# Kernel tuning notes

Measured on AMD Instinct MI355X. Metric: run time of the kernel, lower is better.

The kernel has to match this reference:

```python
import jax, jax.numpy as jnp
import numpy as np

N, DEG, FIN, FOUT, K = 50000, 16, 32, 64, 3
E = N * DEG


def setup_inputs() -> dict:
    key = jax.random.key(0)
    ks = jax.random.split(key, 10)
    rng = np.random.default_rng(0)
    # unique edges sorted row-major (src*N+dst), ring guarantees deg_in/out>0
    ring = np.arange(N, dtype=np.int64) * N + (np.arange(N, dtype=np.int64) + 1) % N
    cand = np.unique(rng.integers(0, N * N, size=3 * E, dtype=np.int64))
    cand = np.setdiff1d(cand, ring, assume_unique=True)[: E - N]
    codes = np.sort(np.concatenate([cand, ring]))
    assert codes.shape[0] == E
    edge_index = jnp.asarray(np.stack([codes // N, codes % N]).astype(np.int32))
    X = jax.random.normal(ks[0], (N, FIN), jnp.float32)
    edge_weight = jax.random.uniform(ks[1], (E,), jnp.float32, 0.5, 1.5)
    cin = FIN + FOUT
    xav = float(np.sqrt(6.0 / (cin + FOUT)))
    def w(k):
        return jax.random.uniform(k, (2, K, cin, FOUT), jnp.float32, -xav, xav)
    return {
        'X': X, 'edge_index': edge_index, 'edge_weight': edge_weight,
        'Wz': w(ks[2]), 'bz': jnp.zeros((FOUT,), jnp.float32),
        'Wr': w(ks[3]), 'br': jnp.zeros((FOUT,), jnp.float32),
        'Wh': w(ks[4]), 'bh': jnp.zeros((FOUT,), jnp.float32),
    }


def _dconv(X, src, dst, rev_src, rev_dst, norm_out, norm_in, W, b):
    n = X.shape[0]
    def prop(x, s, d, nrm):  # out[d] += nrm * x[s]
        return jax.ops.segment_sum(nrm[:, None] * x[s], d, num_segments=n)
    H = X @ W[0, 0] + X @ W[1, 0]
    if W.shape[1] > 1:
        Tx1o = prop(X, src, dst, norm_out)
        Tx1i = prop(X, rev_src, rev_dst, norm_in)
        H = H + Tx1o @ W[0, 1] + Tx1i @ W[1, 1]
        for k in range(2, W.shape[1]):
            Tx1o = 2.0 * prop(Tx1o, src, dst, norm_out) - X
            Tx1i = 2.0 * prop(Tx1i, rev_src, rev_dst, norm_in) - X
            H = H + Tx1o @ W[0, k] + Tx1i @ W[1, k]
    return H + b


def reference(X, edge_index, edge_weight, Wz, bz, Wr, br, Wh, bh):
    n = X.shape[0]
    src, dst = edge_index[0], edge_index[1]
    deg_out = jax.ops.segment_sum(edge_weight, src, num_segments=n)
    deg_in = jax.ops.segment_sum(edge_weight, dst, num_segments=n)
    # faithful to original: both norms indexed by row (source)
    norm_out = 1.0 / deg_out[src]
    norm_in = 1.0 / deg_in[src]
    # reverse edges in dense_to_sparse(adj.T) order: sorted by (dst, src)
    order = jnp.argsort(dst.astype(jnp.int64) * n + src.astype(jnp.int64))
    rev_src, rev_dst = dst[order], src[order]
    H = jnp.zeros((n, Wz.shape[-1]), X.dtype)
    dc = lambda inp, W, b: _dconv(inp, src, dst, rev_src, rev_dst, norm_out, norm_in, W, b)
    Z = jax.nn.sigmoid(dc(jnp.concatenate([X, H], axis=1), Wz, bz))
    R = jax.nn.sigmoid(dc(jnp.concatenate([X, H], axis=1), Wr, br))
    H_tilde = jnp.tanh(dc(jnp.concatenate([X, H * R], axis=1), Wh, bh))
    return Z * H + (1.0 - Z) * H_tilde
```

## Files before the change

kernel.cpp:

```cpp
#include <hip/hip_runtime.h>
#include <hip/hip_fp16.h>
#include <cmath>

#define NN 50000
#define NE 800000
#define PADF 96
#define NBIN 196
#define NBLK 391
#define FCAP 6144
#define DST_HI 42949
#define SRC_CUT 33648

__device__ __forceinline__ unsigned short f2h(float f) {
  __half h = __float2half_rn(f);
  return *reinterpret_cast<unsigned short*>(&h);
}

typedef _Float16 half4 __attribute__((ext_vector_type(4)));
typedef float f32x4 __attribute__((ext_vector_type(4)));

__global__ __launch_bounds__(256) void k_aux(const float* __restrict__ X, const int* __restrict__ src,
                                             const int* __restrict__ dst, const float* __restrict__ ew,
                                             int* __restrict__ H,
                                             int* __restrict__ rptr, float* __restrict__ dout,
                                             const float* __restrict__ Wz, const float* __restrict__ Wh,
                                             unsigned short* __restrict__ WT, unsigned short* __restrict__ Xh) {
  __shared__ int hh[256];
  int bid = blockIdx.x;
  int t = threadIdx.x;
  if (bid >= 667) {
    int h = bid - 667;
    hh[t] = 0;
    __syncthreads();
#pragma unroll
    for (int r = 0; r < 8; ++r) {
      int e = h * 2048 + r * 256 + t;
      if (e < NE) atomicAdd(&hh[dst[e] >> 8], 1);
    }
    __syncthreads();
    if (t < NBIN) H[t * NBLK + h] = hh[t];
  } else if (bid < 196) {
    int i = bid * 256 + t;
    if (i >= NN) return;
    int lo = 0, hi = NE;
    while (lo < hi) { int m = (lo + hi) >> 1; if (src[m] < i) lo = m + 1; else hi = m; }
    int lo2 = lo, hi2 = NE;
    while (lo2 < hi2) { int m = (lo2 + hi2) >> 1; if (src[m] < i + 1) lo2 = m + 1; else hi2 = m; }
    rptr[i] = lo;
    if (i == NN - 1) rptr[NN] = lo2;
    float a = 0.f;
    for (int p = lo; p < lo2; ++p) a += ew[p];
    dout[i] = a;
  } else if (bid < 276) {
    int idx = (bid - 196) * 256 + t;
    int kk = idx >> 7, f = idx & 127;
    int blk = kk >> 5, c = kk & 31;
    const float* W = (f < 64) ? Wz : Wh;
    int fl = f & 63;
    float v;
    if (blk == 0)      v = W[c * 64 + fl] + W[18432 + c * 64 + fl];
    else if (blk == 1) v = W[6144 + c * 64 + fl];
    else if (blk == 2) v = W[18432 + 6144 + c * 64 + fl];
    else if (blk == 3) v = W[2 * 6144 + c * 64 + fl];
    else               v = W[18432 + 2 * 6144 + c * 64 + fl];
    WT[f * 160 + kk] = f2h(v);
  } else {
    int tt = (bid - 276) * 256 + t;
    int base = tt * 16;
    if (base >= NN * 32) return;
#pragma unroll
    for (int q = 0; q < 2; ++q) {
      const float4 a = *(const float4*)&X[base + q * 8];
      const float4 b = *(const float4*)&X[base + q * 8 + 4];
      ushort4 o1 = make_ushort4(f2h(a.x), f2h(a.y), f2h(a.z), f2h(a.w));
      ushort4 o2 = make_ushort4(f2h(b.x), f2h(b.y), f2h(b.z), f2h(b.w));
      *(ushort4*)&Xh[base + q * 8] = o1;
      *(ushort4*)&Xh[base + q * 8 + 4] = o2;
    }
  }
}

__global__ __launch_bounds__(512) void k_scanrow(int* __restrict__ H, int* __restrict__ rowtot) {
  __shared__ int tmp[512];
  int row = blockIdx.x;
  int t = threadIdx.x;
  int v = (t < NBLK) ? H[row * NBLK + t] : 0;
  tmp[t] = v;
  __syncthreads();
  for (int off = 1; off < 512; off <<= 1) {
    int u = (t >= (unsigned)off) ? tmp[t - off] : 0;
    __syncthreads();
    tmp[t] += u;
    __syncthreads();
  }
  if (t < NBLK) H[row * NBLK + t] = tmp[t] - v;
  if (t == 511) rowtot[row] = tmp[511];
}

__global__ __launch_bounds__(256) void k_part(const int* __restrict__ src, const int* __restrict__ dst,
                                              const int* __restrict__ P, const int* __restrict__ rowtot,
                                              unsigned long long* __restrict__ cmp64) {
  __shared__ int loc[NBIN];
  __shared__ int rs[256];
  __shared__ int rbase[NBIN];
  int h = blockIdx.x;
  int t = threadIdx.x;
  int v = (t < NBIN) ? rowtot[t] : 0;
  rs[t] = v;
  if (t < NBIN) loc[t] = 0;
  __syncthreads();
  for (int off = 1; off < 256; off <<= 1) {
    int u = (t >= (unsigned)off) ? rs[t - off] : 0;
    __syncthreads();
    rs[t] += u;
    __syncthreads();
  }
  if (t < NBIN) rbase[t] = rs[t] - v;
  __syncthreads();
#pragma unroll
  for (int r = 0; r < 8; ++r) {
    int e = h * 2048 + r * 256 + t;
    if (e < NE) {
      int d = dst[e];
      int bin = d >> 8;
      int rk = atomicAdd(&loc[bin], 1);
      int pos = rbase[bin] + P[bin * NBLK + h] + rk;
      cmp64[pos] = ((unsigned long long)(d & 255) << 48) |
                   ((unsigned long long)src[e] << 24) | (unsigned long long)e;
    }
  }
}

__global__ __launch_bounds__(1024) void k_fine(const int* __restrict__ rowtot, const float* __restrict__ ew,
                                               const unsigned long long* __restrict__ cmp64,
                                               int2* __restrict__ cmp, int* __restrict__ sp,
                                               float* __restrict__ din) {
  __shared__ unsigned long long a1[FCAP], a2[FCAP];
  __shared__ int fh[256], fcnt[256], fo[257];
  __shared__ int bs[2];
  int cb = blockIdx.x;
  int t = threadIdx.x;
  if (t < 64) {
    int s = 0;
    for (int i = t; i < cb; i += 64) s += rowtot[i];
    s += __shfl_xor(s, 32, 64); s += __shfl_xor(s, 16, 64); s += __shfl_xor(s, 8, 64);
    s += __shfl_xor(s, 4, 64);  s += __shfl_xor(s, 2, 64);  s += __shfl_xor(s, 1, 64);
    if (t == 0) { bs[0] = s; bs[1] = s + rowtot[cb]; }
  }
  if (t < 256) { fh[t] = 0; fcnt[t] = 0; }
  __syncthreads();
  int base = bs[0];
  int m = bs[1] - base;
  if (m > FCAP) m = FCAP;
  for (int i = t; i < m; i += 1024) {
    unsigned long long it = cmp64[base + i];
    a1[i] = it;
    atomicAdd(&fh[(int)(it >> 48)], 1);
  }
  __syncthreads();
  if (t < 64) {
    int v0 = fh[t * 4], v1 = fh[t * 4 + 1], v2 = fh[t * 4 + 2], v3 = fh[t * 4 + 3];
    int s1 = v0 + v1, s2 = s1 + v2, tot = s2 + v3;
    int run = tot;
    for (int off = 1; off < 64; off <<= 1) {
      int v = __shfl_up(run, off, 64);
      if (t >= off) run += v;
    }
    int excl = run - tot;
    fo[t * 4] = excl; fo[t * 4 + 1] = excl + v0; fo[t * 4 + 2] = excl + s1; fo[t * 4 + 3] = excl + s2;
    if (t == 63) fo[256] = excl + tot;
  }
  __syncthreads();
  for (int i = t; i < m; i += 1024) {
    unsigned long long it = a1[i];
    int b = (int)(it >> 48);
    int p2 = fo[b] + atomicAdd(&fcnt[b], 1);
    a2[p2] = it;
  }
  __syncthreads();
  for (int i = t; i < m; i += 1024) {
    unsigned long long it = a2[i];
    cmp[base + i] = make_int2((int)(it & 0xFFFFFF), (int)((it >> 24) & 0xFFFF));
  }
  if (t < 256) {
    int d = cb * 256 + t;
    if (d <= NN) sp[d] = base + fo[t];
  }
  {
    int d = cb * 256 + t;
    if (t < 257 && d == NN) sp[NN] = base + fo[t];
  }
  int nd = t >> 2, ln = t & 3;
  int d = cb * 256 + nd;
  if (d < NN) {
    float s = 0.f;
    int e0 = fo[nd], e1 = fo[nd + 1];
    for (int i = e0 + ln; i < e1; i += 4) s += ew[(int)(a2[i] & 0xFFFFFF)];
    s += __shfl_down(s, 2, 4);
    s += __shfl_down(s, 1, 4);
    if (ln == 0) din[d] = s;
  }
}

__global__ __launch_bounds__(256) void k_sortw(const int* __restrict__ sp, const int2* __restrict__ cmp,
                                               const int* __restrict__ rawsrc,
                                               const float* __restrict__ dout, const float* __restrict__ din,
                                               int2* __restrict__ cnf, int2* __restrict__ cnr) {
  __shared__ int s0s;
  {
    int t = threadIdx.x;
    if (t < 64) {
      int b0h = sp[DST_HI];
      int nh = sp[DST_HI + 1] - b0h;
      int c = 0;
      for (int i = t; i < nh; i += 64) c += (cmp[b0h + i].y < SRC_CUT);
      c += __shfl_xor(c, 32, 64); c += __shfl_xor(c, 16, 64); c += __shfl_xor(c, 8, 64);
      c += __shfl_xor(c, 4, 64);  c += __shfl_xor(c, 2, 64);  c += __shfl_xor(c, 1, 64);
      if (t == 0) s0s = b0h + c;
    }
  }
  __syncthreads();
  int wv = (blockIdx.x * 256 + threadIdx.x) >> 6;
  int lane = threadIdx.x & 63;
  if (wv >= NN) return;
  int b0 = sp[wv], b1 = sp[wv + 1];
  int n = b1 - b0;
  int s0 = s0s;
  if (n > 64) {
    if (lane == 0) {
      int es[PADF], ss[PADF];
      int nn = n > PADF ? PADF : n;
      for (int i = 0; i < nn; ++i) { int2 pe = cmp[b0 + i]; es[i] = pe.x; ss[i] = pe.y; }
      for (int i = 1; i < nn; ++i) {
        int ve = es[i], vs = ss[i]; int j = i - 1;
        while (j >= 0 && es[j] > ve) { es[j + 1] = es[j]; ss[j + 1] = ss[j]; --j; }
        es[j + 1] = ve; ss[j + 1] = vs;
      }
      for (int i = 0; i < nn; ++i) {
        int vs = ss[i];
        cnf[b0 + i] = make_int2(vs, __float_as_int(1.0f / dout[vs]));
        int j = b0 + i - s0; if (j < 0) j += NE;
        cnr[es[i]] = make_int2(wv, __float_as_int(1.0f / din[rawsrc[j]]));
      }
    }
    return;
  }
  unsigned long long k = ~0ULL;
  if (lane < n) {
    int2 pe = cmp[b0 + lane];
    k = ((unsigned long long)(unsigned)pe.x << 32) | (unsigned)pe.y;
  }
  if (n > 1) {
#pragma unroll
    for (int kk = 2; kk <= 64; kk <<= 1) {
#pragma unroll
      for (int j = kk >> 1; j > 0; j >>= 1) {
        unsigned long long o = __shfl_xor(k, j, 64);
        bool lower = (lane & j) == 0;
        bool asc = (lane & kk) == 0;
        bool keepmin = (lower == asc);
        if (keepmin ? (o < k) : (o > k)) k = o;
      }
    }
  }
  if (lane < n) {
    int ve = (int)(k >> 32);
    int vs = (int)(k & 0xffffffffu);
    cnf[b0 + lane] = make_int2(vs, __float_as_int(1.0f / dout[vs]));
    int j = b0 + lane - s0; if (j < 0) j += NE;
    cnr[ve] = make_int2(wv, __float_as_int(1.0f / din[rawsrc[j]]));
  }
}

__global__ __launch_bounds__(256) void k_prop2(const unsigned short* __restrict__ inA, const int* __restrict__ rpA,
                                               const int2* __restrict__ cnA, float* __restrict__ outA,
                                               unsigned short* __restrict__ outAh,
                                               const unsigned short* __restrict__ inB, const int* __restrict__ rpB,
                                               const int2* __restrict__ cnB, float* __restrict__ outB,
                                               unsigned short* __restrict__ outBh,
                                               const float* __restrict__ sub, float mul) {
  int t = blockIdx.x * 256 + threadIdx.x;
  const int half = NN * 8;
  const unsigned short* in; const int* rp; const int2* cn; float* out; unsigned short* outh;
  if (t < half) { in = inA; rp = rpA; cn = cnA; out = outA; outh = outAh; }
  else          { in = inB; rp = rpB; cn = cnB; out = outB; outh = outBh; t -= half; }
  int r = t >> 3;
  if (r >= NN) return;
  int lane8 = t & 7;
  int c4 = lane8 * 4;
  int b = rp[r], e2 = rp[r + 1];
  float a0[4] = {0.f, 0.f, 0.f, 0.f}, a1[4] = {0.f, 0.f, 0.f, 0.f};
  int p = b;
#define GATH(cc, ww) { \
    uint2 bv = *(const uint2*)&in[(cc) * 32 + c4]; \
    float2 f01 = __half22float2(*(const __half2*)&bv.x); \
    float2 f23 = __half22float2(*(const __half2*)&bv.y); \
    float* a = (jj & 1) ? a1 : a0; \
    a[0] += (ww) * f01.x; a[1] += (ww) * f01.y; \
    a[2] += (ww) * f23.x; a[3] += (ww) * f23.y; }
  for (; p + 16 <= e2; p += 16) {
    int2 u = cn[p + lane8];
    int2 v = cn[p + 8 + lane8];
#pragma unroll
    for (int jj = 0; jj < 8; ++jj) {
      int col = __shfl(u.x, jj, 8);
      float w = __int_as_float(__shfl(u.y, jj, 8));
      GATH(col, w)
    }
#pragma unroll
    for (int jj = 0; jj < 8; ++jj) {
      int col = __shfl(v.x, jj, 8);
      float w = __int_as_float(__shfl(v.y, jj, 8));
      GATH(col, w)
    }
  }
  for (; p + 8 <= e2; p += 8) {
    int2 u = cn[p + lane8];
#pragma unroll
    for (int jj = 0; jj < 8; ++jj) {
      int col = __shfl(u.x, jj, 8);
      float w = __int_as_float(__shfl(u.y, jj, 8));
      GATH(col, w)
    }
  }
  for (int jj = 0; p < e2; ++p) {
    int2 c1 = cn[p];
    float w = __int_as_float(c1.y);
    GATH(c1.x, w)
  }
#undef GATH
  float ax = a0[0] + a1[0], ay = a0[1] + a1[1], az = a0[2] + a1[2], aw = a0[3] + a1[3];
  float4 o;
  if (sub) {
    const float4 s = *(const float4*)&sub[r * 32 + c4];
    o.x = mul * ax - s.x; o.y = mul * ay - s.y; o.z = mul * az - s.z; o.w = mul * aw - s.w;
  } else {
    o.x = ax; o.y = ay; o.z = az; o.w = aw;
  }
  if (out) *(float4*)&out[r * 32 + c4] = o;
  if (outh) {
    ushort4 oh = make_ushort4(f2h(o.x), f2h(o.y), f2h(o.z), f2h(o.w));
    *(ushort4*)&outh[r * 32 + c4] = oh;
  }
}

__global__ __launch_bounds__(256) void k_gemm(const unsigned short* __restrict__ Xh,
                                              const unsigned short* __restrict__ T1oh,
                                              const unsigned short* __restrict__ T1ih,
                                              const unsigned short* __restrict__ T2oh,
                                              const unsigned short* __restrict__ T2ih,
                                              const unsigned short* __restrict__ WT,
                                              const float* __restrict__ bz, const float* __restrict__ bh,
                                              float* __restrict__ out) {
  __shared__ unsigned short wlds[128 * 168];
  const int tid = threadIdx.x;
  for (int i = tid; i < 128 * 20; i += 256) {
    int n = i / 20, o = i % 20;
    *(uint4*)&wlds[n * 168 + o * 8] = *(const uint4*)&WT[n * 160 + o * 8];
  }
  __syncthreads();
  const int l = tid & 63, wid = tid >> 6;
  const int m0 = wid * 16;
  const int rb = blockIdx.x * 64;
  int grow = rb + m0 + (l & 15); if (grow >= NN) grow = NN - 1;
  const int kg = (l >> 4) * 4;
  f32x4 acc[8];
#pragma unroll
  for (int t = 0; t < 8; ++t) acc[t] = (f32x4){0.f, 0.f, 0.f, 0.f};
  const unsigned short* srcs[5] = {Xh, T1oh, T1ih, T2oh, T2ih};
#pragma unroll
  for (int s = 0; s < 5; ++s) {
    const unsigned short* A = srcs[s];
#pragma unroll
    for (int h2 = 0; h2 < 2; ++h2) {
      const int kk = h2 * 16;
      half4 af = *(const half4*)&A[grow * 32 + kk + kg];
      const int kglob = s * 32 + kk + kg;
#pragma unroll
      for (int t = 0; t < 8; ++t) {
        half4 bf = *(const half4*)&wlds[(t * 16 + (l & 15)) * 168 + kglob];
        acc[t] = __builtin_amdgcn_mfma_f32_16x16x16f16(af, bf, acc[t], 0, 0, 0);
      }
    }
  }
  const int c = l & 15;
#pragma unroll
  for (int t = 0; t < 4; ++t) {
    int col = t * 16 + c;
    float bzv = bz[col], bhv = bh[col];
#pragma unroll
    for (int i = 0; i < 4; ++i) {
      int r = rb + m0 + (l >> 4) * 4 + i;
      if (r < NN) {
        float z = 1.f / (1.f + expf(-(acc[t][i] + bzv)));
        float hv = tanhf(acc[t + 4][i] + bhv);
        out[r * 64 + col] = (1.f - z) * hv;
      }
    }
  }
}

extern "C" void kernel_launch(void* const* d_in, const int* in_sizes, int n_in,
                              void* d_out, int out_size, void* d_ws, size_t ws_size,
                              hipStream_t stream) {
  const float* X  = (const float*)d_in[0];
  const int*   ei = (const int*)d_in[1];
  const float* ew = (const float*)d_in[2];
  const float* Wz = (const float*)d_in[3];
  const float* bz = (const float*)d_in[4];
  const float* Wh = (const float*)d_in[7];
  const float* bh = (const float*)d_in[8];
  float* out = (float*)d_out;
  const int* src = ei;
  const int* dst = ei + NE;

  char* p = (char*)d_ws;
  auto alloc = [&](size_t bytes) -> char* {
    char* r = p;
    p += (bytes + 255) & ~(size_t)255;
    return r;
  };
  unsigned short* Xh   = (unsigned short*)alloc((size_t)NN * 32 * 2);
  unsigned short* T1oh = (unsigned short*)alloc((size_t)NN * 32 * 2);
  unsigned short* T1ih = (unsigned short*)alloc((size_t)NN * 32 * 2);
  unsigned short* T2oh = (unsigned short*)alloc((size_t)NN * 32 * 2);
  unsigned short* T2ih = (unsigned short*)alloc((size_t)NN * 32 * 2);
  unsigned long long* cmp64 = (unsigned long long*)alloc((size_t)NE * 8);
  int2*  cmp     = (int2*)alloc((size_t)NE * 8);
  int2*  cnf     = (int2*)alloc((size_t)NE * 8);
  int2*  cnr     = (int2*)alloc((size_t)NE * 8);
  int*   H       = (int*)alloc((size_t)NBIN * NBLK * 4);
  int*   rowtot  = (int*)alloc(NBIN * 4);
  int*   sp      = (int*)alloc((NN + 1) * 4);
  int*   rptr    = (int*)alloc((NN + 1) * 4);
  float* dout    = (float*)alloc(NN * 4);
  float* din     = (float*)alloc(NN * 4);
  unsigned short* WT = (unsigned short*)alloc(128 * 160 * 2);

  k_aux<<<1058, 256, 0, stream>>>(X, src, dst, ew, H, rptr, dout, Wz, Wh, WT, Xh);
  k_scanrow<<<NBIN, 512, 0, stream>>>(H, rowtot);
  k_part<<<NBLK, 256, 0, stream>>>(src, dst, H, rowtot, cmp64);
  k_fine<<<NBIN, 1024, 0, stream>>>(rowtot, ew, cmp64, cmp, sp, din);
  k_sortw<<<12500, 256, 0, stream>>>(sp, cmp, src, dout, din, cnf, cnr);

  k_prop2<<<3125, 256, 0, stream>>>(Xh, sp, cnf, nullptr, T1oh,
                                    Xh, rptr, cnr, nullptr, T1ih, nullptr, 1.f);
  k_prop2<<<3125, 256, 0, stream>>>(T1oh, sp, cnf, nullptr, T2oh,
                                    T1ih, rptr, cnr, nullptr, T2ih, X, 2.f);

  k_gemm<<<782, 256, 0, stream>>>(Xh, T1oh, T1ih, T2oh, T2ih, WT, bz, bh, out);
}
```

Baseline: 233.4 us.

## Fuse per-destination edge sort into k_fine and defer in-degree reciprocal to propagation

```diff
diff --git a/kernel.cpp b/kernel.cpp
--- a/kernel.cpp
+++ b/kernel.cpp
@@ -24,21 +24,32 @@
                                              int* __restrict__ H,
                                              int* __restrict__ rptr, float* __restrict__ dout,
                                              const float* __restrict__ Wz, const float* __restrict__ Wh,
-                                             unsigned short* __restrict__ WT, unsigned short* __restrict__ Xh) {
+                                             unsigned short* __restrict__ WT, unsigned short* __restrict__ Xh,
+                                             int* __restrict__ s0g) {
   __shared__ int hh[256];
+  __shared__ int s0l;
   int bid = blockIdx.x;
   int t = threadIdx.x;
   if (bid >= 667) {
     int h = bid - 667;
     hh[t] = 0;
-    __syncthreads();
+    if (t == 0) s0l = 0;
+    __syncthreads();
+    int my = 0;
 #pragma unroll
     for (int r = 0; r < 8; ++r) {
       int e = h * 2048 + r * 256 + t;
-      if (e < NE) atomicAdd(&hh[dst[e] >> 8], 1);
-    }
+      if (e < NE) {
+        int d = dst[e];
+        atomicAdd(&hh[d >> 8], 1);
+        my += (d < DST_HI) ? 1 : 0;
+        my += (d == DST_HI && src[e] < SRC_CUT) ? 1 : 0;
+      }
+    }
+    atomicAdd(&s0l, my);
     __syncthreads();
     if (t < NBIN) H[t * NBLK + h] = hh[t];
+    if (t == 0) atomicAdd(s0g, s0l);
   } else if (bid < 196) {
     int i = bid * 256 + t;
     if (i >= NN) return;
@@ -133,8 +144,10 @@
 
 __global__ __launch_bounds__(1024) void k_fine(const int* __restrict__ rowtot, const float* __restrict__ ew,
                                                const unsigned long long* __restrict__ cmp64,
-                                               int2* __restrict__ cmp, int* __restrict__ sp,
-                                               float* __restrict__ din) {
+                                               const int* __restrict__ rawsrc, const float* __restrict__ dout,
+                                               const int* __restrict__ s0g,
+                                               int* __restrict__ sp, float* __restrict__ din,
+                                               int2* __restrict__ cnf, int2* __restrict__ cnr) {
   __shared__ unsigned long long a1[FCAP], a2[FCAP];
   __shared__ int fh[256], fcnt[256], fo[257];
   __shared__ int bs[2];
@@ -177,11 +190,6 @@
     int p2 = fo[b] + atomicAdd(&fcnt[b], 1);
     a2[p2] = it;
   }
-  __syncthreads();
-  for (int i = t; i < m; i += 1024) {
-    unsigned long long it = a2[i];
-    cmp[base + i] = make_int2((int)(it & 0xFFFFFF), (int)((it >> 24) & 0xFFFF));
-  }
   if (t < 256) {
     int d = cb * 256 + t;
     if (d <= NN) sp[d] = base + fo[t];
@@ -190,100 +198,82 @@
     int d = cb * 256 + t;
     if (t < 257 && d == NN) sp[NN] = base + fo[t];
   }
-  int nd = t >> 2, ln = t & 3;
-  int d = cb * 256 + nd;
-  if (d < NN) {
-    float s = 0.f;
-    int e0 = fo[nd], e1 = fo[nd + 1];
-    for (int i = e0 + ln; i < e1; i += 4) s += ew[(int)(a2[i] & 0xFFFFFF)];
-    s += __shfl_down(s, 2, 4);
-    s += __shfl_down(s, 1, 4);
-    if (ln == 0) din[d] = s;
-  }
-}
-
-__global__ __launch_bounds__(256) void k_sortw(const int* __restrict__ sp, const int2* __restrict__ cmp,
-                                               const int* __restrict__ rawsrc,
-                                               const float* __restrict__ dout, const float* __restrict__ din,
-                                               int2* __restrict__ cnf, int2* __restrict__ cnr) {
-  __shared__ int s0s;
-  {
-    int t = threadIdx.x;
-    if (t < 64) {
-      int b0h = sp[DST_HI];
-      int nh = sp[DST_HI + 1] - b0h;
-      int c = 0;
-      for (int i = t; i < nh; i += 64) c += (cmp[b0h + i].y < SRC_CUT);
-      c += __shfl_xor(c, 32, 64); c += __shfl_xor(c, 16, 64); c += __shfl_xor(c, 8, 64);
-      c += __shfl_xor(c, 4, 64);  c += __shfl_xor(c, 2, 64);  c += __shfl_xor(c, 1, 64);
-      if (t == 0) s0s = b0h + c;
-    }
-  }
-  __syncthreads();
-  int wv = (blockIdx.x * 256 + threadIdx.x) >> 6;
-  int lane = threadIdx.x & 63;
-  if (wv >= NN) return;
-  int b0 = sp[wv], b1 = sp[wv + 1];
-  int n = b1 - b0;
-  int s0 = s0s;
-  if (n > 64) {
-    if (lane == 0) {
-      int es[PADF], ss[PADF];
-      int nn = n > PADF ? PADF : n;
-      for (int i = 0; i < nn; ++i) { int2 pe = cmp[b0 + i]; es[i] = pe.x; ss[i] = pe.y; }
-      for (int i = 1; i < nn; ++i) {
-        int ve = es[i], vs = ss[i]; int j = i - 1;
-        while (j >= 0 && es[j] > ve) { es[j + 1] = es[j]; ss[j + 1] = ss[j]; --j; }
-        es[j + 1] = ve; ss[j + 1] = vs;
+  __syncthreads();
+  const int s0 = s0g[0];
+  const int wv0 = t >> 6, lane = t & 63;
+  for (int seg = wv0; seg < 256; seg += 16) {
+    int d = cb * 256 + seg;
+    if (d >= NN) break;
+    int f0 = fo[seg], f1 = fo[seg + 1];
+    int n = f1 - f0;
+    int b0g = base + f0;
+    if (n > 64) {
+      if (lane == 0) {
+        unsigned long long arr[PADF];
+        int nn = n > PADF ? PADF : n;
+        for (int i = 0; i < nn; ++i) arr[i] = a2[f0 + i];
+        for (int i = 1; i < nn; ++i) {
+          unsigned long long v = arr[i]; int j = i - 1;
+          while (j >= 0 && arr[j] > v) { arr[j + 1] = arr[j]; --j; }
+          arr[j + 1] = v;
+        }
+        float s = 0.f;
+        for (int i = 0; i < nn; ++i) {
+          unsigned long long it = arr[i];
+          int e = (int)(it & 0xFFFFFF);
+          int sc = (int)((it >> 24) & 0xFFFF);
+          s += ew[e];
+          cnf[b0g + i] = make_int2(sc, __float_as_int(1.0f / dout[sc]));
+          int j = b0g + i - s0; if (j < 0) j += NE;
+          cnr[e] = make_int2(d, rawsrc[j]);
+        }
+        din[d] = s;
       }
-      for (int i = 0; i < nn; ++i) {
-        int vs = ss[i];
-        cnf[b0 + i] = make_int2(vs, __float_as_int(1.0f / dout[vs]));
-        int j = b0 + i - s0; if (j < 0) j += NE;
-        cnr[es[i]] = make_int2(wv, __float_as_int(1.0f / din[rawsrc[j]]));
+      continue;
+    }
+    unsigned long long k = ~0ULL;
+    if (lane < n) k = a2[f0 + lane];
+    if (n > 1) {
+#pragma unroll
+      for (int kk = 2; kk <= 64; kk <<= 1) {
+#pragma unroll
+        for (int j = kk >> 1; j > 0; j >>= 1) {
+          unsigned long long o = __shfl_xor(k, j, 64);
+          bool lower = (lane & j) == 0;
+          bool asc = (lane & kk) == 0;
+          bool keepmin = (lower == asc);
+          if (keepmin ? (o < k) : (o > k)) k = o;
+        }
       }
     }
-    return;
-  }
-  unsigned long long k = ~0ULL;
-  if (lane < n) {
-    int2 pe = cmp[b0 + lane];
-    k = ((unsigned long long)(unsigned)pe.x << 32) | (unsigned)pe.y;
-  }
-  if (n > 1) {
-#pragma unroll
-    for (int kk = 2; kk <= 64; kk <<= 1) {
-#pragma unroll
-      for (int j = kk >> 1; j > 0; j >>= 1) {
-        unsigned long long o = __shfl_xor(k, j, 64);
-        bool lower = (lane & j) == 0;
-        bool asc = (lane & kk) == 0;
-        bool keepmin = (lower == asc);
-        if (keepmin ? (o < k) : (o > k)) k = o;
-      }
-    }
-  }
-  if (lane < n) {
-    int ve = (int)(k >> 32);
-    int vs = (int)(k & 0xffffffffu);
-    cnf[b0 + lane] = make_int2(vs, __float_as_int(1.0f / dout[vs]));
-    int j = b0 + lane - s0; if (j < 0) j += NE;
-    cnr[ve] = make_int2(wv, __float_as_int(1.0f / din[rawsrc[j]]));
+    float wsum = 0.f;
+    if (lane < n) {
+      int e = (int)(k & 0xFFFFFF);
+      int sc = (int)((k >> 24) & 0xFFFF);
+      wsum = ew[e];
+      cnf[b0g + lane] = make_int2(sc, __float_as_int(1.0f / dout[sc]));
+      int j = b0g + lane - s0; if (j < 0) j += NE;
+      cnr[e] = make_int2(d, rawsrc[j]);
+    }
+    wsum += __shfl_xor(wsum, 32, 64); wsum += __shfl_xor(wsum, 16, 64);
+    wsum += __shfl_xor(wsum, 8, 64);  wsum += __shfl_xor(wsum, 4, 64);
+    wsum += __shfl_xor(wsum, 2, 64);  wsum += __shfl_xor(wsum, 1, 64);
+    if (lane == 0) din[d] = wsum;
   }
 }
 
 __global__ __launch_bounds__(256) void k_prop2(const unsigned short* __restrict__ inA, const int* __restrict__ rpA,
-                                               const int2* __restrict__ cnA, float* __restrict__ outA,
+                                               const int2* __restrict__ cnA, const float* __restrict__ wiA,
                                                unsigned short* __restrict__ outAh,
                                                const unsigned short* __restrict__ inB, const int* __restrict__ rpB,
-                                               const int2* __restrict__ cnB, float* __restrict__ outB,
+                                               const int2* __restrict__ cnB, const float* __restrict__ wiB,
                                                unsigned short* __restrict__ outBh,
                                                const float* __restrict__ sub, float mul) {
   int t = blockIdx.x * 256 + threadIdx.x;
   const int half = NN * 8;
-  const unsigned short* in; const int* rp; const int2* cn; float* out; unsigned short* outh;
-  if (t < half) { in = inA; rp = rpA; cn = cnA; out = outA; outh = outAh; }
-  else          { in = inB; rp = rpB; cn = cnB; out = outB; outh = outBh; t -= half; }
+  const unsigned short* in; const int* rp; const int2* cn; const float* wi; unsigned short* outh;
+  if (t < half) { in = inA; rp = rpA; cn = cnA; wi = wiA; outh = outAh; }
+  else          { in = inB; rp = rpB; cn = cnB; wi = wiB; outh = outBh; t -= half; }
   int r = t >> 3;
   if (r >= NN) return;
   int lane8 = t & 7;
@@ -301,31 +291,34 @@
   for (; p + 16 <= e2; p += 16) {
     int2 u = cn[p + lane8];
     int2 v = cn[p + 8 + lane8];
+    float uw = wi ? (1.0f / wi[u.y]) : __int_as_float(u.y);
+    float vw = wi ? (1.0f / wi[v.y]) : __int_as_float(v.y);
 #pragma unroll
     for (int jj = 0; jj < 8; ++jj) {
       int col = __shfl(u.x, jj, 8);
-      float w = __int_as_float(__shfl(u.y, jj, 8));
+      float w = __shfl(uw, jj, 8);
       GATH(col, w)
     }
 #pragma unroll
     for (int jj = 0; jj < 8; ++jj) {
       int col = __shfl(v.x, jj, 8);
-      float w = __int_as_float(__shfl(v.y, jj, 8));
+      float w = __shfl(vw, jj, 8);
       GATH(col, w)
     }
   }
   for (; p + 8 <= e2; p += 8) {
     int2 u = cn[p + lane8];
+    float uw = wi ? (1.0f / wi[u.y]) : __int_as_float(u.y);
 #pragma unroll
     for (int jj = 0; jj < 8; ++jj) {
       int col = __shfl(u.x, jj, 8);
-      float w = __int_as_float(__shfl(u.y, jj, 8));
+      float w = __shfl(uw, jj, 8);
       GATH(col, w)
     }
   }
   for (int jj = 0; p < e2; ++p) {
     int2 c1 = cn[p];
-    float w = __int_as_float(c1.y);
+    float w = wi ? (1.0f / wi[c1.y]) : __int_as_float(c1.y);
     GATH(c1.x, w)
   }
 #undef GATH
@@ -337,11 +330,8 @@
   } else {
     o.x = ax; o.y = ay; o.z = az; o.w = aw;
   }
-  if (out) *(float4*)&out[r * 32 + c4] = o;
-  if (outh) {
-    ushort4 oh = make_ushort4(f2h(o.x), f2h(o.y), f2h(o.z), f2h(o.w));
-    *(ushort4*)&outh[r * 32 + c4] = oh;
-  }
+  ushort4 oh = make_ushort4(f2h(o.x), f2h(o.y), f2h(o.z), f2h(o.w));
+  *(ushort4*)&outh[r * 32 + c4] = oh;
 }
 
 __global__ __launch_bounds__(256) void k_gemm(const unsigned short* __restrict__ Xh,
@@ -426,7 +416,6 @@
   unsigned short* T2oh = (unsigned short*)alloc((size_t)NN * 32 * 2);
   unsigned short* T2ih = (unsigned short*)alloc((size_t)NN * 32 * 2);
   unsigned long long* cmp64 = (unsigned long long*)alloc((size_t)NE * 8);
-  int2*  cmp     = (int2*)alloc((size_t)NE * 8);
   int2*  cnf     = (int2*)alloc((size_t)NE * 8);
   int2*  cnr     = (int2*)alloc((size_t)NE * 8);
   int*   H       = (int*)alloc((size_t)NBIN * NBLK * 4);
@@ -436,17 +425,18 @@
   float* dout    = (float*)alloc(NN * 4);
   float* din     = (float*)alloc(NN * 4);
   unsigned short* WT = (unsigned short*)alloc(128 * 160 * 2);
-
-  k_aux<<<1058, 256, 0, stream>>>(X, src, dst, ew, H, rptr, dout, Wz, Wh, WT, Xh);
+  int*   s0g     = (int*)alloc(256);
+
+  hipMemsetAsync(s0g, 0, 4, stream);
+  k_aux<<<1058, 256, 0, stream>>>(X, src, dst, ew, H, rptr, dout, Wz, Wh, WT, Xh, s0g);
   k_scanrow<<<NBIN, 512, 0, stream>>>(H, rowtot);
   k_part<<<NBLK, 256, 0, stream>>>(src, dst, H, rowtot, cmp64);
-  k_fine<<<NBIN, 1024, 0, stream>>>(rowtot, ew, cmp64, cmp, sp, din);
-  k_sortw<<<12500, 256, 0, stream>>>(sp, cmp, src, dout, din, cnf, cnr);
+  k_fine<<<NBIN, 1024, 0, stream>>>(rowtot, ew, cmp64, src, dout, s0g, sp, din, cnf, cnr);
 
   k_prop2<<<3125, 256, 0, stream>>>(Xh, sp, cnf, nullptr, T1oh,
-                                    Xh, rptr, cnr, nullptr, T1ih, nullptr, 1.f);
+                                    Xh, rptr, cnr, din, T1ih, nullptr, 1.f);
   k_prop2<<<3125, 256, 0, stream>>>(T1oh, sp, cnf, nullptr, T2oh,
-                                    T1ih, rptr, cnr, nullptr, T2ih, X, 2.f);
+                                    T1ih, rptr, cnr, din, T2ih, X, 2.f);
 
   k_gemm<<<782, 256, 0, stream>>>(Xh, T1oh, T1ih, T2oh, T2ih, WT, bz, bh, out);
 }
```

Result: slower. 258.9 us (+11.0%).
